# Kernel optimization log

Measured on AMD Instinct MI355X. Metric: run time of the kernel, lower is better.

Reference implementation:

```python
import jax, jax.numpy as jnp
import numpy as np

B, N, DIM = 4, 4096, 1024
HEADS, DIM_HEAD, M = 16, 64, 128
DIM_INNER = HEADS * DIM_HEAD
SCALE = DIM_HEAD ** -0.5


def setup_inputs() -> dict:
    key = jax.random.key(0)
    ks = jax.random.split(key, 7)
    x = jax.random.normal(ks[0], (B, N, DIM), dtype=jnp.float32)
    mask = jax.random.bernoulli(ks[1], 0.9, (B, N))  # bool [b, n]
    W_qkv = jax.random.normal(ks[2], (DIM, 3 * DIM_INNER), dtype=jnp.float32) * (DIM ** -0.5)
    agent_tokens = jax.random.normal(ks[3], (HEADS, M, DIM_HEAD), dtype=jnp.float32) * 0.02
    W_qa = jax.random.normal(ks[4], (HEADS, HEADS), dtype=jnp.float32) * (HEADS ** -0.5)
    W_ak = jax.random.normal(ks[5], (HEADS, HEADS), dtype=jnp.float32) * (HEADS ** -0.5)
    W_out = jax.random.normal(ks[6], (DIM_INNER, DIM), dtype=jnp.float32) * (DIM_INNER ** -0.5)
    return {"x": x, "mask": mask, "W_qkv": W_qkv, "agent_tokens": agent_tokens,
            "W_qa": W_qa, "W_ak": W_ak, "W_out": W_out}


def reference(x, mask, W_qkv, agent_tokens, W_qa, W_ak, W_out):
    b, n, _ = x.shape
    h, m, d = agent_tokens.shape
    # qkv projection -> [3, b, h, n, d]  (layout matches 'b n (qkv h d)')
    qkv = (x @ W_qkv).reshape(b, n, 3, h, d).transpose(2, 0, 3, 1, 4)
    q, k, v = qkv[0], qkv[1], qkv[2]
    a = agent_tokens * SCALE  # [h, m, d]
    # stage 1: query-agent similarities [b, h, n, m]
    qa_sim = jnp.einsum('bhid,hjd->bhij', q, a)
    # stage 2: agent-key similarities [b, h, m, n]
    ak_sim = jnp.einsum('hid,bhjd->bhij', a, k)
    max_neg = -jnp.finfo(ak_sim.dtype).max
    ak_sim = jnp.where(mask[:, None, None, :], ak_sim, max_neg)
    qa_attn = jax.nn.softmax(qa_sim, axis=-1)
    ak_attn = jax.nn.softmax(ak_sim, axis=-1)
    # talking heads: 1x1 conv over head dim == head-mixing matmul
    qa_attn = jnp.einsum('gh,bhij->bgij', W_qa, qa_attn)
    ak_attn = jnp.einsum('gh,bhij->bgij', W_ak, ak_attn)
    agent_out = jnp.einsum('bhmn,bhnd->bhmd', ak_attn, v)    # [b, h, m, d]
    out = jnp.einsum('bhnm,bhmd->bhnd', qa_attn, agent_out)  # [b, h, n, d]
    out = jnp.where(mask[:, None, :, None], out, 0.0)
    out = out.transpose(0, 2, 1, 3).reshape(b, n, h * d)
    return out @ W_out
```

## Files before the change

kernel.cpp:

```cpp
#include <hip/hip_runtime.h>
#include <stdint.h>

#define DEVI __device__ __forceinline__

typedef __bf16 bf16x8 __attribute__((ext_vector_type(8)));
typedef float  f32x4  __attribute__((ext_vector_type(4)));
typedef unsigned int u32x2 __attribute__((ext_vector_type(2)));


DEVI unsigned short f2bf(float f) {
  union { float f; unsigned int u; } c; c.f = f;
  return (unsigned short)((c.u + 0x7fffu + ((c.u >> 16) & 1u)) >> 16);
}
DEVI float bf2f(unsigned short s) {
  union { unsigned int u; float f; } c; c.u = ((unsigned int)s) << 16;
  return c.f;
}
DEVI u32x2 pack4(float a, float b, float c, float d) {
  u32x2 r;
  r.x = (unsigned)f2bf(a) | ((unsigned)f2bf(b) << 16);
  r.y = (unsigned)f2bf(c) | ((unsigned)f2bf(d) << 16);
  return r;
}
DEVI bf16x8 ldg8(const unsigned short* p) { return *(const bf16x8*)p; }

DEVI void g2l16(const void* g, void* l) {
  __builtin_amdgcn_global_load_lds(
      (const __attribute__((address_space(1))) unsigned int*)g,
      (__attribute__((address_space(3))) unsigned int*)l, 16, 0, 0);
}

#define MFMA16(acc, a, b) acc = __builtin_amdgcn_mfma_f32_16x16x32_bf16((a), (b), (acc), 0, 0, 0)

#define VMCNT8() asm volatile("s_waitcnt vmcnt(8)")
#define VMCNT0() asm volatile("s_waitcnt vmcnt(0)")
#define LGKM0()  asm volatile("s_waitcnt lgkmcnt(0)")
#define SBAR()   __builtin_amdgcn_s_barrier()

__global__ __launch_bounds__(256) void k_prep(
    const float* __restrict__ x, const float* __restrict__ Wqkv,
    const float* __restrict__ ag, const float* __restrict__ Wout,
    unsigned short* __restrict__ Xb, unsigned short* __restrict__ WqkvT,
    unsigned short* __restrict__ Ab, unsigned short* __restrict__ WoT,
    float* __restrict__ rowsum)
{
  __shared__ float ldsT[32][33];
  const int tid = threadIdx.x;
  int bx = blockIdx.x;
  if (bx < 16384) {
    size_t i4 = ((size_t)bx * 256 + tid) * 4;
    f32x4 v = *(const f32x4*)&x[i4];
    *(u32x2*)&Xb[i4] = pack4(v[0], v[1], v[2], v[3]);
    return;
  }
  bx -= 16384;
  if (bx < 3072) {
    int jt = bx % 96, kt = bx / 96;
    int r32 = tid >> 3, c4 = (tid & 7) * 4;
    f32x4 v = *(const f32x4*)&Wqkv[(size_t)(kt * 32 + r32) * 3072 + jt * 32 + c4];
#pragma unroll
    for (int i = 0; i < 4; i++) ldsT[r32][c4 + i] = v[i];
    __syncthreads();
    float o0 = ldsT[c4 + 0][r32], o1 = ldsT[c4 + 1][r32];
    float o2 = ldsT[c4 + 2][r32], o3 = ldsT[c4 + 3][r32];
    *(u32x2*)&WqkvT[(size_t)(jt * 32 + r32) * 1024 + kt * 32 + c4] = pack4(o0, o1, o2, o3);
    return;
  }
  bx -= 3072;
  if (bx < 128) {
    size_t i4 = ((size_t)bx * 256 + tid) * 4;
    f32x4 v = *(const f32x4*)&ag[i4];
    *(u32x2*)&Ab[i4] = pack4(v[0] * 0.125f, v[1] * 0.125f, v[2] * 0.125f, v[3] * 0.125f);
    return;
  }
  bx -= 128;
  if (bx < 1024) {
    int ct = bx % 32, dt = bx / 32;
    int r32 = tid >> 3, c4 = (tid & 7) * 4;
    f32x4 v = *(const f32x4*)&Wout[(size_t)(dt * 32 + r32) * 1024 + ct * 32 + c4];
#pragma unroll
    for (int i = 0; i < 4; i++) ldsT[r32][c4 + i] = v[i];
    __syncthreads();
    float o0 = ldsT[c4 + 0][r32], o1 = ldsT[c4 + 1][r32];
    float o2 = ldsT[c4 + 2][r32], o3 = ldsT[c4 + 3][r32];
    *(u32x2*)&WoT[(size_t)(ct * 32 + r32) * 1024 + dt * 32 + c4] = pack4(o0, o1, o2, o3);
    return;
  }
  bx -= 1024;
  {
    const f32x4 z = {0.f, 0.f, 0.f, 0.f};
    *(f32x4*)&rowsum[((size_t)bx * 256 + tid) * 4] = z;
  }
}

DEVI void gemm_core_256(const unsigned short* __restrict__ A,
                        const unsigned short* __restrict__ Bt,
                        int row0, int col0, int swap,
                        unsigned short* ldsS, f32x4 acc[8][4])
{
  const int tid = threadIdx.x, lane = tid & 63, w = tid >> 6;
  const int q = lane >> 4, r = lane & 15;
  const int wm = w >> 2, wn = w & 3;
  const int abA = swap ? 2 : 0, abB = swap ? 0 : 2;
  const int afhalf = wm, bvhalf = wn >> 1;
  const int afr = r * 64;
  const int bvr = ((wn & 1) * 64 + r) * 64;
  const int cs0 = (q ^ (r & 7)) << 3;
  const int cs1 = ((q + 4) ^ (r & 7)) << 3;
  const int gr = tid >> 3;
  const int gcol = ((tid & 7) ^ ((tid >> 3) & 7)) << 3;
  const unsigned short* gA = A + (size_t)(row0 + gr) * 1024 + gcol;
  const unsigned short* gB = Bt + (size_t)(col0 + gr) * 1024 + gcol;
  const int ldst = w * 512;

  const f32x4 z = {0.f, 0.f, 0.f, 0.f};
#pragma unroll
  for (int i = 0; i < 8; i++)
#pragma unroll
    for (int j = 0; j < 4; j++) acc[i][j] = z;

  auto stageH = [&](const unsigned short* G, int half, int koff, int slot) {
    const unsigned short* g0 = G + (size_t)half * 131072 + koff;
    g2l16(g0, ldsS + slot + ldst);
    g2l16(g0 + 65536, ldsS + slot + 4096 + ldst);
  };

#pragma unroll
  for (int s = 0; s < 2; ++s) {
    stageH(gB, 0, s * 64, ((s << 2) | 2 | 0) << 13);
    stageH(gB, 1, s * 64, ((s << 2) | 2 | 1) << 13);
    stageH(gA, 0, s * 64, ((s << 2) | 0 | 0) << 13);
    stageH(gA, 1, s * 64, ((s << 2) | 0 | 1) << 13);
  }
  VMCNT8();
  SBAR();

  auto kstep = [&](const int P, const int s) {
    const int afb = (((P << 2) | abA | afhalf) << 13) + afr;
    const int bvb = (((P << 2) | abB | bvhalf) << 13) + bvr;
    bf16x8 af[4][2], bva[2][2], bvx[2][2];
#pragma unroll
    for (int rt = 0; rt < 4; rt++) {
      af[rt][0] = *(const bf16x8*)&ldsS[afb + rt * 1024 + cs0];
      af[rt][1] = *(const bf16x8*)&ldsS[afb + rt * 1024 + cs1];
    }
#pragma unroll
    for (int ct = 0; ct < 2; ct++) {
      bva[ct][0] = *(const bf16x8*)&ldsS[bvb + ct * 1024 + cs0];
      bva[ct][1] = *(const bf16x8*)&ldsS[bvb + ct * 1024 + cs1];
    }
    SBAR(); LGKM0();
    __builtin_amdgcn_s_setprio(1);
#pragma unroll
    for (int rt = 0; rt < 4; rt++)
#pragma unroll
      for (int ct = 0; ct < 2; ct++) {
        MFMA16(acc[rt][ct], af[rt][0], bva[ct][0]);
        MFMA16(acc[rt][ct], af[rt][1], bva[ct][1]);
      }
    __builtin_amdgcn_s_setprio(0);
    SBAR();
#pragma unroll
    for (int ct = 0; ct < 2; ct++) {
      bvx[ct][0] = *(const bf16x8*)&ldsS[bvb + (ct + 2) * 1024 + cs0];
      bvx[ct][1] = *(const bf16x8*)&ldsS[bvb + (ct + 2) * 1024 + cs1];
    }
    SBAR(); LGKM0();
    __builtin_amdgcn_s_setprio(1);
#pragma unroll
    for (int rt = 0; rt < 4; rt++)
#pragma unroll
      for (int ct = 0; ct < 2; ct++) {
        MFMA16(acc[rt][ct + 2], af[rt][0], bvx[ct][0]);
        MFMA16(acc[rt][ct + 2], af[rt][1], bvx[ct][1]);
      }
    __builtin_amdgcn_s_setprio(0);
    SBAR();
#pragma unroll
    for (int rt = 0; rt < 4; rt++) {
      af[rt][0] = *(const bf16x8*)&ldsS[afb + (rt + 4) * 1024 + cs0];
      af[rt][1] = *(const bf16x8*)&ldsS[afb + (rt + 4) * 1024 + cs1];
    }
    if (s < 14) {
      stageH(gB, 0, (s + 2) * 64, ((P << 2) | 2 | 0) << 13);
      stageH(gB, 1, (s + 2) * 64, ((P << 2) | 2 | 1) << 13);
    }
    SBAR(); LGKM0();
    __builtin_amdgcn_s_setprio(1);
#pragma unroll
    for (int rt = 0; rt < 4; rt++)
#pragma unroll
      for (int ct = 0; ct < 2; ct++) {
        MFMA16(acc[rt + 4][ct], af[rt][0], bva[ct][0]);
        MFMA16(acc[rt + 4][ct], af[rt][1], bva[ct][1]);
      }
    __builtin_amdgcn_s_setprio(0);
    SBAR();
    if (s < 14) {
      stageH(gA, 0, (s + 2) * 64, ((P << 2) | 0 | 0) << 13);
      stageH(gA, 1, (s + 2) * 64, ((P << 2) | 0 | 1) << 13);
      VMCNT8();
    } else if (s == 14) {
      VMCNT0();
    }
    SBAR(); LGKM0();
    __builtin_amdgcn_s_setprio(1);
#pragma unroll
    for (int rt = 0; rt < 4; rt++)
#pragma unroll
      for (int ct = 0; ct < 2; ct++) {
        MFMA16(acc[rt + 4][ct + 2], af[rt][0], bvx[ct][0]);
        MFMA16(acc[rt + 4][ct + 2], af[rt][1], bvx[ct][1]);
      }
    __builtin_amdgcn_s_setprio(0);
    SBAR();
  };

  for (int it = 0; it < 8; ++it) {
    kstep(0, 2 * it);
    kstep(1, 2 * it + 1);
  }
}

__global__ __launch_bounds__(512, 2) void k_gemm_qkv(
    const unsigned short* __restrict__ A, const unsigned short* __restrict__ Bt,
    unsigned short* __restrict__ Q, unsigned short* __restrict__ Kd,
    unsigned short* __restrict__ Vt)
{
  __shared__ __align__(16) unsigned short lds[65536];
  const int tid = threadIdx.x, lane = tid & 63, w = tid >> 6;
  const int q = lane >> 4, r = lane & 15, wm = w >> 2, wn = w & 3;
  const int row0 = blockIdx.x * 256, col0 = blockIdx.y * 256;
  const bool qk = blockIdx.y < 8;

  f32x4 acc[8][4];
  gemm_core_256(A, Bt, row0, col0, qk ? 1 : 0, lds, acc);

  const int b = row0 >> 12, row0b = row0 & 4095;
  if (qk) {
    unsigned short* dst = (col0 < 1024) ? Q : Kd;
    const int jb = (col0 & 1023) + wm * 128;
#pragma unroll
    for (int rt = 0; rt < 8; rt++)
#pragma unroll
      for (int ct = 0; ct < 4; ct++) {
        int j = jb + rt * 16 + 4 * q;
        int h = j >> 6, d0 = j & 63;
        int n = row0b + wn * 64 + ct * 16 + r;
        u32x2 pk = pack4(acc[rt][ct][0], acc[rt][ct][1], acc[rt][ct][2], acc[rt][ct][3]);
        *(u32x2*)&dst[(((size_t)(b * 16 + h)) * 4096 + n) * 64 + d0] = pk;
      }
  } else {
    const int jb = (col0 - 2048) + wn * 64;
#pragma unroll
    for (int rt = 0; rt < 8; rt++)
#pragma unroll
      for (int ct = 0; ct < 4; ct++) {
        int j = jb + ct * 16 + r;
        int h = j >> 6, d = j & 63;
        int n = row0b + wm * 128 + rt * 16 + 4 * q;
        u32x2 pk = pack4(acc[rt][ct][0], acc[rt][ct][1], acc[rt][ct][2], acc[rt][ct][3]);
        *(u32x2*)&Vt[(((size_t)(b * 16 + h)) * 64 + d) * 4096 + n] = pk;
      }
  }
}

__global__ __launch_bounds__(256, 2) void k_qk(
    const unsigned short* __restrict__ Q, const unsigned short* __restrict__ Kd,
    const unsigned short* __restrict__ Ab, const int* __restrict__ mask,
    unsigned short* __restrict__ QA, unsigned short* __restrict__ E,
    float* __restrict__ rowsum)
{
  const int tid = threadIdx.x, lane = tid & 63, w = tid >> 6;
  const int q = lane >> 4, r = lane & 15, wr = w >> 1, wc = w & 1;
  const int nt = blockIdx.x, h = blockIdx.y, b = blockIdx.z;
  const unsigned short* Qb = Q + (((size_t)(b * 16 + h)) * 4096 + nt * 128) * 64;
  const unsigned short* Kb = Kd + (((size_t)(b * 16 + h)) * 4096 + nt * 128) * 64;
  const unsigned short* Ah = Ab + (size_t)h * 8192;
  __shared__ float rs[2][128];
  const f32x4 z = {0.f, 0.f, 0.f, 0.f};

  {
    f32x4 acc[4][4];
#pragma unroll
    for (int i = 0; i < 4; i++)
#pragma unroll
      for (int j = 0; j < 4; j++) acc[i][j] = z;
#pragma unroll
    for (int ks = 0; ks < 2; ks++) {
      bf16x8 af[4], bv[4];
#pragma unroll
      for (int rt = 0; rt < 4; rt++) af[rt] = ldg8(Ah + (size_t)(64 * wr + 16 * rt + r) * 64 + ks * 32 + q * 8);
#pragma unroll
      for (int ct = 0; ct < 4; ct++) bv[ct] = ldg8(Qb + (size_t)(64 * wc + 16 * ct + r) * 64 + ks * 32 + q * 8);
#pragma unroll
      for (int rt = 0; rt < 4; rt++)
#pragma unroll
        for (int ct = 0; ct < 4; ct++) MFMA16(acc[rt][ct], af[rt], bv[ct]);
    }
    float cs[4];
#pragma unroll
    for (int ct = 0; ct < 4; ct++) {
      float s = 0.f;
#pragma unroll
      for (int rt = 0; rt < 4; rt++)
#pragma unroll
        for (int reg = 0; reg < 4; reg++) {
          float e = __expf(acc[rt][ct][reg]);
          acc[rt][ct][reg] = e; s += e;
        }
      s += __shfl_xor(s, 16); s += __shfl_xor(s, 32);
      cs[ct] = s;
    }
    if (q == 0) {
#pragma unroll
      for (int ct = 0; ct < 4; ct++) rs[wr][64 * wc + 16 * ct + r] = cs[ct];
    }
    __syncthreads();
#pragma unroll
    for (int ct = 0; ct < 4; ct++) {
      int nl = 64 * wc + 16 * ct + r;
      float inv = 1.0f / (rs[0][nl] + rs[1][nl]);
      int n = nt * 128 + nl;
      size_t base = (((size_t)(b * 16 + h)) * 4096 + n) * 128;
#pragma unroll
      for (int rt = 0; rt < 4; rt++) {
        int m0 = 64 * wr + 16 * rt + 4 * q;
        u32x2 pk = pack4(acc[rt][ct][0] * inv, acc[rt][ct][1] * inv,
                         acc[rt][ct][2] * inv, acc[rt][ct][3] * inv);
        *(u32x2*)&QA[base + m0] = pk;
      }
    }
  }
  __syncthreads();

  {
    f32x4 acc[4][4];
#pragma unroll
    for (int i = 0; i < 4; i++)
#pragma unroll
      for (int j = 0; j < 4; j++) acc[i][j] = z;
#pragma unroll
    for (int ks = 0; ks < 2; ks++) {
      bf16x8 af[4], bv[4];
#pragma unroll
      for (int rt = 0; rt < 4; rt++) af[rt] = ldg8(Kb + (size_t)(64 * wr + 16 * rt + r) * 64 + ks * 32 + q * 8);
#pragma unroll
      for (int ct = 0; ct < 4; ct++) bv[ct] = ldg8(Ah + (size_t)(64 * wc + 16 * ct + r) * 64 + ks * 32 + q * 8);
#pragma unroll
      for (int rt = 0; rt < 4; rt++)
#pragma unroll
        for (int ct = 0; ct < 4; ct++) MFMA16(acc[rt][ct], af[rt], bv[ct]);
    }
    float cs[4] = {0.f, 0.f, 0.f, 0.f};
#pragma unroll
    for (int rt = 0; rt < 4; rt++) {
      const int4 mkv = *(const int4*)&mask[b * 4096 + nt * 128 + 64 * wr + 16 * rt + 4 * q];
      int mka[4] = {mkv.x, mkv.y, mkv.z, mkv.w};
#pragma unroll
      for (int ct = 0; ct < 4; ct++) {
#pragma unroll
        for (int reg = 0; reg < 4; reg++) {
          float e = mka[reg] ? __expf(acc[rt][ct][reg]) : 0.0f;
          acc[rt][ct][reg] = e; cs[ct] += e;
        }
      }
    }
#pragma unroll
    for (int ct = 0; ct < 4; ct++) {
      float s = cs[ct];
      s += __shfl_xor(s, 16); s += __shfl_xor(s, 32);
      cs[ct] = s;
    }
    if (q == 0) {
#pragma unroll
      for (int ct = 0; ct < 4; ct++) rs[wr][64 * wc + 16 * ct + r] = cs[ct];
    }
#pragma unroll
    for (int ct = 0; ct < 4; ct++) {
      int m = 64 * wc + 16 * ct + r;
      size_t base = (((size_t)(b * 16 + h)) * 128 + m) * 4096;
#pragma unroll
      for (int rt = 0; rt < 4; rt++) {
        int n0 = nt * 128 + 64 * wr + 16 * rt + 4 * q;
        u32x2 pk = pack4(acc[rt][ct][0], acc[rt][ct][1], acc[rt][ct][2], acc[rt][ct][3]);
        *(u32x2*)&E[base + n0] = pk;
      }
    }
    __syncthreads();
    if (tid < 128) atomicAdd(&rowsum[(b * 16 + h) * 128 + tid], rs[0][tid] + rs[1][tid]);
  }
}

__global__ __launch_bounds__(256) void k_mix(
    const unsigned short* __restrict__ E, const float* __restrict__ rowsum,
    const float* __restrict__ Wak, unsigned short* __restrict__ MIX)
{
  const int tid = threadIdx.x;
  const int m = blockIdx.y, b = blockIdx.z;
  __shared__ float wv[256];
  __shared__ float inv[16];
  wv[tid] = Wak[tid];
  if (tid < 16) inv[tid] = 1.0f / rowsum[(b * 16 + tid) * 128 + m];
  __syncthreads();
  const int n0 = (blockIdx.x * 256 + tid) * 4;
  float p[16][4];
#pragma unroll
  for (int h = 0; h < 16; h++) {
    u32x2 v = *(const u32x2*)&E[(((size_t)(b * 16 + h)) * 128 + m) * 4096 + n0];
    float iv = inv[h];
    p[h][0] = bf2f((unsigned short)(v.x & 0xffff)) * iv;
    p[h][1] = bf2f((unsigned short)(v.x >> 16)) * iv;
    p[h][2] = bf2f((unsigned short)(v.y & 0xffff)) * iv;
    p[h][3] = bf2f((unsigned short)(v.y >> 16)) * iv;
  }
#pragma unroll
  for (int g = 0; g < 16; g++) {
    float s0 = 0.f, s1 = 0.f, s2 = 0.f, s3 = 0.f;
#pragma unroll
    for (int h = 0; h < 16; h++) {
      float wgh = wv[g * 16 + h];
      s0 += wgh * p[h][0]; s1 += wgh * p[h][1]; s2 += wgh * p[h][2]; s3 += wgh * p[h][3];
    }
    *(u32x2*)&MIX[(((size_t)(b * 16 + g)) * 128 + m) * 4096 + n0] = pack4(s0, s1, s2, s3);
  }
}

__global__ __launch_bounds__(256) void k_ao(
    const unsigned short* __restrict__ MIX, const unsigned short* __restrict__ Vt,
    float* __restrict__ P)
{
  const int tid = threadIdx.x, lane = tid & 63, w4 = tid >> 6;
  const int q = lane >> 4, r = lane & 15;
  const int kc = blockIdx.x, g = blockIdx.y, b = blockIdx.z;
  const unsigned short* Abase = MIX + ((size_t)(b * 16 + g)) * 128 * 4096;
  const unsigned short* Bbase = Vt + ((size_t)(b * 16 + g)) * 64 * 4096;
  f32x4 acc[2][4];
  const f32x4 z = {0.f, 0.f, 0.f, 0.f};
#pragma unroll
  for (int i = 0; i < 2; i++)
#pragma unroll
    for (int j = 0; j < 4; j++) acc[i][j] = z;
  for (int n = kc * 512; n < kc * 512 + 512; n += 32) {
    bf16x8 af[2], bv[4];
#pragma unroll
    for (int rt = 0; rt < 2; rt++) af[rt] = ldg8(Abase + (size_t)(32 * w4 + 16 * rt + r) * 4096 + n + q * 8);
#pragma unroll
    for (int ct = 0; ct < 4; ct++) bv[ct] = ldg8(Bbase + (size_t)(16 * ct + r) * 4096 + n + q * 8);
#pragma unroll
    for (int rt = 0; rt < 2; rt++)
#pragma unroll
      for (int ct = 0; ct < 4; ct++) MFMA16(acc[rt][ct], af[rt], bv[ct]);
  }
  float* Pp = P + (size_t)kc * 524288 + ((size_t)(b * 16 + g)) * 8192;
#pragma unroll
  for (int rt = 0; rt < 2; rt++)
#pragma unroll
    for (int ct = 0; ct < 4; ct++) {
      int m0 = 32 * w4 + 16 * rt + 4 * q, d = 16 * ct + r;
      *(f32x4*)&Pp[(size_t)d * 128 + m0] = acc[rt][ct];
    }
}

__global__ __launch_bounds__(256) void k_aored(
    const float* __restrict__ P, float* __restrict__ AOt)
{
  size_t i = ((size_t)blockIdx.x * 256 + threadIdx.x) * 4;
  f32x4 s = *(const f32x4*)&P[i];
#pragma unroll
  for (int kc = 1; kc < 8; kc++) {
    f32x4 v = *(const f32x4*)&P[(size_t)kc * 524288 + i];
    s[0] += v[0]; s[1] += v[1]; s[2] += v[2]; s[3] += v[3];
  }
  *(f32x4*)&AOt[i] = s;
}

__global__ __launch_bounds__(256) void k_mixqa(
    const unsigned short* __restrict__ QA, const float* __restrict__ Wqa,
    unsigned short* __restrict__ QAmix)
{
  const int tid = threadIdx.x;
  const int b = blockIdx.y;
  __shared__ float wv[256];
  wv[tid] = Wqa[tid];
  __syncthreads();
  const size_t i0 = ((size_t)blockIdx.x * 256 + tid) * 4;
  float p[16][4];
#pragma unroll
  for (int h = 0; h < 16; h++) {
    u32x2 v = *(const u32x2*)&QA[((size_t)(b * 16 + h)) * 524288 + i0];
    p[h][0] = bf2f((unsigned short)(v.x & 0xffff));
    p[h][1] = bf2f((unsigned short)(v.x >> 16));
    p[h][2] = bf2f((unsigned short)(v.y & 0xffff));
    p[h][3] = bf2f((unsigned short)(v.y >> 16));
  }
#pragma unroll
  for (int g = 0; g < 16; g++) {
    float s0 = 0.f, s1 = 0.f, s2 = 0.f, s3 = 0.f;
#pragma unroll
    for (int h = 0; h < 16; h++) {
      float wgh = wv[g * 16 + h];
      s0 += wgh * p[h][0]; s1 += wgh * p[h][1]; s2 += wgh * p[h][2]; s3 += wgh * p[h][3];
    }
    *(u32x2*)&QAmix[((size_t)(b * 16 + g)) * 524288 + i0] = pack4(s0, s1, s2, s3);
  }
}

__global__ __launch_bounds__(256) void k_o1(
    const unsigned short* __restrict__ QAmix, const float* __restrict__ AOt,
    unsigned short* __restrict__ out1)
{
  const int tid = threadIdx.x, lane = tid & 63, w4 = tid >> 6;
  const int q = lane >> 4, r = lane & 15;
  const int nt = blockIdx.x, g = blockIdx.y, b = blockIdx.z;
  const unsigned short* Bbase = QAmix + (((size_t)(b * 16 + g)) * 4096 + nt * 128) * 128;
  const float* Abase = AOt + ((size_t)(b * 16 + g)) * 8192;
  f32x4 acc[4][2];
  const f32x4 z = {0.f, 0.f, 0.f, 0.f};
#pragma unroll
  for (int i = 0; i < 4; i++)
#pragma unroll
    for (int j = 0; j < 2; j++) acc[i][j] = z;
#pragma unroll
  for (int ks = 0; ks < 4; ks++) {
    bf16x8 af[4], bv[2];
#pragma unroll
    for (int rt = 0; rt < 4; rt++) {
      const float* p = Abase + (size_t)(16 * rt + r) * 128 + ks * 32 + q * 8;
      f32x4 f0 = *(const f32x4*)p;
      f32x4 f1 = *(const f32x4*)(p + 4);
      bf16x8 t;
#pragma unroll
      for (int jj = 0; jj < 4; jj++) { t[jj] = (__bf16)f0[jj]; t[4 + jj] = (__bf16)f1[jj]; }
      af[rt] = t;
    }
#pragma unroll
    for (int ct = 0; ct < 2; ct++)
      bv[ct] = ldg8(Bbase + (size_t)(32 * w4 + 16 * ct + r) * 128 + ks * 32 + q * 8);
#pragma unroll
    for (int rt = 0; rt < 4; rt++)
#pragma unroll
      for (int ct = 0; ct < 2; ct++) MFMA16(acc[rt][ct], af[rt], bv[ct]);
  }
#pragma unroll
  for (int ct = 0; ct < 2; ct++) {
    int n = nt * 128 + 32 * w4 + 16 * ct + r;
    size_t base = ((size_t)b * 4096 + n) * 1024 + g * 64;
#pragma unroll
    for (int rt = 0; rt < 4; rt++) {
      int d0 = 16 * rt + 4 * q;
      u32x2 pk = pack4(acc[rt][ct][0], acc[rt][ct][1], acc[rt][ct][2], acc[rt][ct][3]);
      *(u32x2*)&out1[base + d0] = pk;
    }
  }
}

__global__ __launch_bounds__(512, 2) void k_fin2(
    const unsigned short* __restrict__ A, const unsigned short* __restrict__ Bt,
    const int* __restrict__ mask, float* __restrict__ out)
{
  __shared__ __align__(16) unsigned short lds[65536];
  const int tid = threadIdx.x, lane = tid & 63, w = tid >> 6;
  const int q = lane >> 4, r = lane & 15, wm = w >> 2, wn = w & 3;
  const int row0 = blockIdx.x * 256, col0 = blockIdx.y * 256;

  f32x4 acc[8][4];
  gemm_core_256(A, Bt, row0, col0, 0, lds, acc);

#pragma unroll
  for (int rt = 0; rt < 8; rt++) {
    const int4 mkv = *(const int4*)&mask[row0 + wm * 128 + rt * 16 + 4 * q];
    int mka[4] = {mkv.x, mkv.y, mkv.z, mkv.w};
#pragma unroll
    for (int reg = 0; reg < 4; reg++) {
      int row = row0 + wm * 128 + rt * 16 + 4 * q + reg;
#pragma unroll
      for (int ct = 0; ct < 4; ct++) {
        int c = col0 + wn * 64 + ct * 16 + r;
        out[(size_t)row * 1024 + c] = mka[reg] ? acc[rt][ct][reg] : 0.0f;
      }
    }
  }
}

extern "C" void kernel_launch(void* const* d_in, const int* in_sizes, int n_in,
                              void* d_out, int out_size, void* d_ws, size_t ws_size,
                              hipStream_t stream) {
  const float* x    = (const float*)d_in[0];
  const int*   mask = (const int*)d_in[1];
  const float* Wqkv = (const float*)d_in[2];
  const float* ag   = (const float*)d_in[3];
  const float* Wqa  = (const float*)d_in[4];
  const float* Wak  = (const float*)d_in[5];
  const float* Wout = (const float*)d_in[6];
  float* out = (float*)d_out;
  char* ws = (char*)d_ws;

  unsigned short* QA    = (unsigned short*)(ws + 0);
  unsigned short* QQ    = (unsigned short*)(ws + 67108864);
  unsigned short* KK    = (unsigned short*)(ws + 67108864 + 33554432);
  unsigned short* MIX   = QQ;
  unsigned short* out1  = QQ;
  unsigned short* VT    = (unsigned short*)(ws + 134217728);
  unsigned short* Xb    = (unsigned short*)(ws + 167772160);
  unsigned short* WqkvT = (unsigned short*)(ws + 167772160 + 33554432);
  unsigned short* E     = Xb;
  float*          Ppart = (float*)Xb;
  unsigned short* QAmix = Xb;
  char* sm = ws + 234881024;
  unsigned short* Ab  = (unsigned short*)(sm);
  unsigned short* WoT = (unsigned short*)(sm + 262144);
  float* rowsum = (float*)(sm + 262144 + 2097152);
  float* AOt    = (float*)(sm + 262144 + 2097152 + 32768);

  k_prep<<<20616, 256, 0, stream>>>(x, Wqkv, ag, Wout, Xb, WqkvT, Ab, WoT, rowsum);
  k_gemm_qkv<<<dim3(64, 12), 512, 0, stream>>>(Xb, WqkvT, QQ, KK, VT);
  k_qk<<<dim3(32, 16, 4), 256, 0, stream>>>(QQ, KK, Ab, mask, QA, E, rowsum);
  k_mix<<<dim3(4, 128, 4), 256, 0, stream>>>(E, rowsum, Wak, MIX);
  k_ao<<<dim3(8, 16, 4), 256, 0, stream>>>(MIX, VT, Ppart);
  k_aored<<<512, 256, 0, stream>>>(Ppart, AOt);
  k_mixqa<<<dim3(512, 4), 256, 0, stream>>>(QA, Wqa, QAmix);
  k_o1<<<dim3(32, 16, 4), 256, 0, stream>>>(QAmix, AOt, out1);
  k_fin2<<<dim3(64, 4), 512, 0, stream>>>(out1, WoT, mask, out);
}
```

Before: 462.8 us.

## Fuse query-agent softmax with talking-heads mix into one kernel

Adds a new kernel that computes the query-agent similarities for all 16 heads of a 32-row tile, applies the softmax, keeps the bf16 probabilities in registers, and applies the W_qa head mix before writing QAmix. This removes the separate k_mixqa pass and the write and re-read of the 64 MB intermediate QA buffer. k_qk now only handles the agent-key branch. The fused kernel keeps a large register array (16x2x2 packed values plus accumulators), which may lower occupancy. It also needs two block barriers per head and launches only 512 blocks.

```diff
diff --git a/kernel.cpp b/kernel.cpp
--- a/kernel.cpp
+++ b/kernel.cpp
@@ -265,131 +265,181 @@
   }
 }
 
+__global__ __launch_bounds__(256, 2) void k_qamix(
+    const unsigned short* __restrict__ Q, const unsigned short* __restrict__ Ab,
+    const float* __restrict__ Wqa, unsigned short* __restrict__ QAmix)
+{
+  const int tid = threadIdx.x, lane = tid & 63, w = tid >> 6;
+  const int q = lane >> 4, r = lane & 15;
+  const int nt = blockIdx.x, b = blockIdx.y;
+  __shared__ float wq[256];
+  __shared__ float rsq[4][32];
+  wq[tid] = Wqa[tid];
+  __syncthreads();
+
+  const f32x4 z = {0.f, 0.f, 0.f, 0.f};
+  u32x2 p[16][2][2];
+
+#pragma unroll
+  for (int h = 0; h < 16; ++h) {
+    const unsigned short* Qb = Q + (((size_t)(b * 16 + h)) * 4096 + nt * 32) * 64;
+    const unsigned short* Ah = Ab + (size_t)h * 8192;
+    f32x4 acc[2][2];
+    acc[0][0] = z; acc[0][1] = z; acc[1][0] = z; acc[1][1] = z;
+#pragma unroll
+    for (int ks = 0; ks < 2; ++ks) {
+      bf16x8 af[2], bv[2];
+#pragma unroll
+      for (int rt = 0; rt < 2; rt++) af[rt] = ldg8(Ah + (size_t)(32 * w + 16 * rt + r) * 64 + ks * 32 + q * 8);
+#pragma unroll
+      for (int ct = 0; ct < 2; ct++) bv[ct] = ldg8(Qb + (size_t)(16 * ct + r) * 64 + ks * 32 + q * 8);
+#pragma unroll
+      for (int rt = 0; rt < 2; rt++)
+#pragma unroll
+        for (int ct = 0; ct < 2; ct++) MFMA16(acc[rt][ct], af[rt], bv[ct]);
+    }
+    float e[2][2][4];
+    float s0 = 0.f, s1 = 0.f;
+#pragma unroll
+    for (int rt = 0; rt < 2; rt++)
+#pragma unroll
+      for (int reg = 0; reg < 4; reg++) {
+        float e0 = __expf(acc[rt][0][reg]); e[rt][0][reg] = e0; s0 += e0;
+        float e1 = __expf(acc[rt][1][reg]); e[rt][1][reg] = e1; s1 += e1;
+      }
+    s0 += __shfl_xor(s0, 16); s0 += __shfl_xor(s0, 32);
+    s1 += __shfl_xor(s1, 16); s1 += __shfl_xor(s1, 32);
+    if (lane < 16) { rsq[w][r] = s0; rsq[w][16 + r] = s1; }
+    __syncthreads();
+    float invv[2];
+#pragma unroll
+    for (int ct = 0; ct < 2; ct++) {
+      int n = 16 * ct + r;
+      invv[ct] = 1.0f / (rsq[0][n] + rsq[1][n] + rsq[2][n] + rsq[3][n]);
+    }
+#pragma unroll
+    for (int rt = 0; rt < 2; rt++)
+#pragma unroll
+      for (int ct = 0; ct < 2; ct++)
+        p[h][rt][ct] = pack4(e[rt][ct][0] * invv[ct], e[rt][ct][1] * invv[ct],
+                             e[rt][ct][2] * invv[ct], e[rt][ct][3] * invv[ct]);
+    __syncthreads();
+  }
+
+#pragma unroll
+  for (int gg = 0; gg < 4; ++gg) {
+    f32x4 s[4][2][2];
+#pragma unroll
+    for (int gp = 0; gp < 4; gp++) { s[gp][0][0] = z; s[gp][0][1] = z; s[gp][1][0] = z; s[gp][1][1] = z; }
+#pragma unroll
+    for (int h = 0; h < 16; ++h) {
+      float f[2][2][4];
+#pragma unroll
+      for (int rt = 0; rt < 2; rt++)
+#pragma unroll
+        for (int ct = 0; ct < 2; ct++) {
+          u32x2 v = p[h][rt][ct];
+          f[rt][ct][0] = bf2f((unsigned short)(v.x & 0xffff));
+          f[rt][ct][1] = bf2f((unsigned short)(v.x >> 16));
+          f[rt][ct][2] = bf2f((unsigned short)(v.y & 0xffff));
+          f[rt][ct][3] = bf2f((unsigned short)(v.y >> 16));
+        }
+#pragma unroll
+      for (int gp = 0; gp < 4; ++gp) {
+        float wgh = wq[(gg * 4 + gp) * 16 + h];
+#pragma unroll
+        for (int rt = 0; rt < 2; rt++)
+#pragma unroll
+          for (int ct = 0; ct < 2; ct++)
+#pragma unroll
+            for (int reg = 0; reg < 4; reg++)
+              s[gp][rt][ct][reg] += wgh * f[rt][ct][reg];
+      }
+    }
+#pragma unroll
+    for (int gp = 0; gp < 4; ++gp) {
+      int g = gg * 4 + gp;
+      size_t gbase = ((size_t)(b * 16 + g)) * 4096 + nt * 32;
+#pragma unroll
+      for (int rt = 0; rt < 2; rt++)
+#pragma unroll
+        for (int ct = 0; ct < 2; ct++) {
+          int n = 16 * ct + r, m0 = 32 * w + 16 * rt + 4 * q;
+          u32x2 pk = pack4(s[gp][rt][ct][0], s[gp][rt][ct][1],
+                           s[gp][rt][ct][2], s[gp][rt][ct][3]);
+          *(u32x2*)&QAmix[(gbase + n) * 128 + m0] = pk;
+        }
+    }
+  }
+}
+
 __global__ __launch_bounds__(256, 2) void k_qk(
-    const unsigned short* __restrict__ Q, const unsigned short* __restrict__ Kd,
-    const unsigned short* __restrict__ Ab, const int* __restrict__ mask,
-    unsigned short* __restrict__ QA, unsigned short* __restrict__ E,
+    const unsigned short* __restrict__ Kd, const unsigned short* __restrict__ Ab,
+    const int* __restrict__ mask, unsigned short* __restrict__ E,
     float* __restrict__ rowsum)
 {
   const int tid = threadIdx.x, lane = tid & 63, w = tid >> 6;
   const int q = lane >> 4, r = lane & 15, wr = w >> 1, wc = w & 1;
   const int nt = blockIdx.x, h = blockIdx.y, b = blockIdx.z;
-  const unsigned short* Qb = Q + (((size_t)(b * 16 + h)) * 4096 + nt * 128) * 64;
   const unsigned short* Kb = Kd + (((size_t)(b * 16 + h)) * 4096 + nt * 128) * 64;
   const unsigned short* Ah = Ab + (size_t)h * 8192;
   __shared__ float rs[2][128];
   const f32x4 z = {0.f, 0.f, 0.f, 0.f};
 
-  {
-    f32x4 acc[4][4];
-#pragma unroll
-    for (int i = 0; i < 4; i++)
-#pragma unroll
-      for (int j = 0; j < 4; j++) acc[i][j] = z;
-#pragma unroll
-    for (int ks = 0; ks < 2; ks++) {
-      bf16x8 af[4], bv[4];
-#pragma unroll
-      for (int rt = 0; rt < 4; rt++) af[rt] = ldg8(Ah + (size_t)(64 * wr + 16 * rt + r) * 64 + ks * 32 + q * 8);
-#pragma unroll
-      for (int ct = 0; ct < 4; ct++) bv[ct] = ldg8(Qb + (size_t)(64 * wc + 16 * ct + r) * 64 + ks * 32 + q * 8);
-#pragma unroll
-      for (int rt = 0; rt < 4; rt++)
-#pragma unroll
-        for (int ct = 0; ct < 4; ct++) MFMA16(acc[rt][ct], af[rt], bv[ct]);
-    }
-    float cs[4];
+  f32x4 acc[4][4];
+#pragma unroll
+  for (int i = 0; i < 4; i++)
+#pragma unroll
+    for (int j = 0; j < 4; j++) acc[i][j] = z;
+#pragma unroll
+  for (int ks = 0; ks < 2; ks++) {
+    bf16x8 af[4], bv[4];
+#pragma unroll
+    for (int rt = 0; rt < 4; rt++) af[rt] = ldg8(Kb + (size_t)(64 * wr + 16 * rt + r) * 64 + ks * 32 + q * 8);
+#pragma unroll
+    for (int ct = 0; ct < 4; ct++) bv[ct] = ldg8(Ah + (size_t)(64 * wc + 16 * ct + r) * 64 + ks * 32 + q * 8);
+#pragma unroll
+    for (int rt = 0; rt < 4; rt++)
+#pragma unroll
+      for (int ct = 0; ct < 4; ct++) MFMA16(acc[rt][ct], af[rt], bv[ct]);
+  }
+  float cs[4] = {0.f, 0.f, 0.f, 0.f};
+#pragma unroll
+  for (int rt = 0; rt < 4; rt++) {
+    const int4 mkv = *(const int4*)&mask[b * 4096 + nt * 128 + 64 * wr + 16 * rt + 4 * q];
+    int mka[4] = {mkv.x, mkv.y, mkv.z, mkv.w};
 #pragma unroll
     for (int ct = 0; ct < 4; ct++) {
-      float s = 0.f;
-#pragma unroll
-      for (int rt = 0; rt < 4; rt++)
-#pragma unroll
-        for (int reg = 0; reg < 4; reg++) {
-          float e = __expf(acc[rt][ct][reg]);
-          acc[rt][ct][reg] = e; s += e;
-        }
-      s += __shfl_xor(s, 16); s += __shfl_xor(s, 32);
-      cs[ct] = s;
-    }
-    if (q == 0) {
-#pragma unroll
-      for (int ct = 0; ct < 4; ct++) rs[wr][64 * wc + 16 * ct + r] = cs[ct];
-    }
-    __syncthreads();
-#pragma unroll
-    for (int ct = 0; ct < 4; ct++) {
-      int nl = 64 * wc + 16 * ct + r;
-      float inv = 1.0f / (rs[0][nl] + rs[1][nl]);
-      int n = nt * 128 + nl;
-      size_t base = (((size_t)(b * 16 + h)) * 4096 + n) * 128;
-#pragma unroll
-      for (int rt = 0; rt < 4; rt++) {
-        int m0 = 64 * wr + 16 * rt + 4 * q;
-        u32x2 pk = pack4(acc[rt][ct][0] * inv, acc[rt][ct][1] * inv,
-                         acc[rt][ct][2] * inv, acc[rt][ct][3] * inv);
-        *(u32x2*)&QA[base + m0] = pk;
-      }
+#pragma unroll
+      for (int reg = 0; reg < 4; reg++) {
+        float e = mka[reg] ? __expf(acc[rt][ct][reg]) : 0.0f;
+        acc[rt][ct][reg] = e; cs[ct] += e;
+      }
+    }
+  }
+#pragma unroll
+  for (int ct = 0; ct < 4; ct++) {
+    float s = cs[ct];
+    s += __shfl_xor(s, 16); s += __shfl_xor(s, 32);
+    cs[ct] = s;
+  }
+  if (q == 0) {
+#pragma unroll
+    for (int ct = 0; ct < 4; ct++) rs[wr][64 * wc + 16 * ct + r] = cs[ct];
+  }
+#pragma unroll
+  for (int ct = 0; ct < 4; ct++) {
+    int m = 64 * wc + 16 * ct + r;
+    size_t base = (((size_t)(b * 16 + h)) * 128 + m) * 4096;
+#pragma unroll
+    for (int rt = 0; rt < 4; rt++) {
+      int n0 = nt * 128 + 64 * wr + 16 * rt + 4 * q;
+      u32x2 pk = pack4(acc[rt][ct][0], acc[rt][ct][1], acc[rt][ct][2], acc[rt][ct][3]);
+      *(u32x2*)&E[base + n0] = pk;
     }
   }
   __syncthreads();
-
-  {
-    f32x4 acc[4][4];
-#pragma unroll
-    for (int i = 0; i < 4; i++)
-#pragma unroll
-      for (int j = 0; j < 4; j++) acc[i][j] = z;
-#pragma unroll
-    for (int ks = 0; ks < 2; ks++) {
-      bf16x8 af[4], bv[4];
-#pragma unroll
-      for (int rt = 0; rt < 4; rt++) af[rt] = ldg8(Kb + (size_t)(64 * wr + 16 * rt + r) * 64 + ks * 32 + q * 8);
-#pragma unroll
-      for (int ct = 0; ct < 4; ct++) bv[ct] = ldg8(Ah + (size_t)(64 * wc + 16 * ct + r) * 64 + ks * 32 + q * 8);
-#pragma unroll
-      for (int rt = 0; rt < 4; rt++)
-#pragma unroll
-        for (int ct = 0; ct < 4; ct++) MFMA16(acc[rt][ct], af[rt], bv[ct]);
-    }
-    float cs[4] = {0.f, 0.f, 0.f, 0.f};
-#pragma unroll
-    for (int rt = 0; rt < 4; rt++) {
-      const int4 mkv = *(const int4*)&mask[b * 4096 + nt * 128 + 64 * wr + 16 * rt + 4 * q];
-      int mka[4] = {mkv.x, mkv.y, mkv.z, mkv.w};
-#pragma unroll
-      for (int ct = 0; ct < 4; ct++) {
-#pragma unroll
-        for (int reg = 0; reg < 4; reg++) {
-          float e = mka[reg] ? __expf(acc[rt][ct][reg]) : 0.0f;
-          acc[rt][ct][reg] = e; cs[ct] += e;
-        }
-      }
-    }
-#pragma unroll
-    for (int ct = 0; ct < 4; ct++) {
-      float s = cs[ct];
-      s += __shfl_xor(s, 16); s += __shfl_xor(s, 32);
-      cs[ct] = s;
-    }
-    if (q == 0) {
-#pragma unroll
-      for (int ct = 0; ct < 4; ct++) rs[wr][64 * wc + 16 * ct + r] = cs[ct];
-    }
-#pragma unroll
-    for (int ct = 0; ct < 4; ct++) {
-      int m = 64 * wc + 16 * ct + r;
-      size_t base = (((size_t)(b * 16 + h)) * 128 + m) * 4096;
-#pragma unroll
-      for (int rt = 0; rt < 4; rt++) {
-        int n0 = nt * 128 + 64 * wr + 16 * rt + 4 * q;
-        u32x2 pk = pack4(acc[rt][ct][0], acc[rt][ct][1], acc[rt][ct][2], acc[rt][ct][3]);
-        *(u32x2*)&E[base + n0] = pk;
-      }
-    }
-    __syncthreads();
-    if (tid < 128) atomicAdd(&rowsum[(b * 16 + h) * 128 + tid], rs[0][tid] + rs[1][tid]);
-  }
+  if (tid < 128) atomicAdd(&rowsum[(b * 16 + h) * 128 + tid], rs[0][tid] + rs[1][tid]);
 }
 
 __global__ __launch_bounds__(256) void k_mix(
@@ -473,37 +523,6 @@
     s[0] += v[0]; s[1] += v[1]; s[2] += v[2]; s[3] += v[3];
   }
   *(f32x4*)&AOt[i] = s;
-}
-
-__global__ __launch_bounds__(256) void k_mixqa(
-    const unsigned short* __restrict__ QA, const float* __restrict__ Wqa,
-    unsigned short* __restrict__ QAmix)
-{
-  const int tid = threadIdx.x;
-  const int b = blockIdx.y;
-  __shared__ float wv[256];
-  wv[tid] = Wqa[tid];
-  __syncthreads();
-  const size_t i0 = ((size_t)blockIdx.x * 256 + tid) * 4;
-  float p[16][4];
-#pragma unroll
-  for (int h = 0; h < 16; h++) {
-    u32x2 v = *(const u32x2*)&QA[((size_t)(b * 16 + h)) * 524288 + i0];
-    p[h][0] = bf2f((unsigned short)(v.x & 0xffff));
-    p[h][1] = bf2f((unsigned short)(v.x >> 16));
-    p[h][2] = bf2f((unsigned short)(v.y & 0xffff));
-    p[h][3] = bf2f((unsigned short)(v.y >> 16));
-  }
-#pragma unroll
-  for (int g = 0; g < 16; g++) {
-    float s0 = 0.f, s1 = 0.f, s2 = 0.f, s3 = 0.f;
-#pragma unroll
-    for (int h = 0; h < 16; h++) {
-      float wgh = wv[g * 16 + h];
-      s0 += wgh * p[h][0]; s1 += wgh * p[h][1]; s2 += wgh * p[h][2]; s3 += wgh * p[h][3];
-    }
-    *(u32x2*)&QAmix[((size_t)(b * 16 + g)) * 524288 + i0] = pack4(s0, s1, s2, s3);
-  }
 }
 
 __global__ __launch_bounds__(256) void k_o1(
@@ -596,7 +615,7 @@
   float* out = (float*)d_out;
   char* ws = (char*)d_ws;
 
-  unsigned short* QA    = (unsigned short*)(ws + 0);
+  unsigned short* QAmix = (unsigned short*)(ws + 0);
   unsigned short* QQ    = (unsigned short*)(ws + 67108864);
   unsigned short* KK    = (unsigned short*)(ws + 67108864 + 33554432);
   unsigned short* MIX   = QQ;
@@ -606,7 +625,6 @@
   unsigned short* WqkvT = (unsigned short*)(ws + 167772160 + 33554432);
   unsigned short* E     = Xb;
   float*          Ppart = (float*)Xb;
-  unsigned short* QAmix = Xb;
   char* sm = ws + 234881024;
   unsigned short* Ab  = (unsigned short*)(sm);
   unsigned short* WoT = (unsigned short*)(sm + 262144);
@@ -615,11 +633,11 @@
 
   k_prep<<<20616, 256, 0, stream>>>(x, Wqkv, ag, Wout, Xb, WqkvT, Ab, WoT, rowsum);
   k_gemm_qkv<<<dim3(64, 12), 512, 0, stream>>>(Xb, WqkvT, QQ, KK, VT);
-  k_qk<<<dim3(32, 16, 4), 256, 0, stream>>>(QQ, KK, Ab, mask, QA, E, rowsum);
+  k_qamix<<<dim3(128, 4), 256, 0, stream>>>(QQ, Ab, Wqa, QAmix);
+  k_qk<<<dim3(32, 16, 4), 256, 0, stream>>>(KK, Ab, mask, E, rowsum);
   k_mix<<<dim3(4, 128, 4), 256, 0, stream>>>(E, rowsum, Wak, MIX);
   k_ao<<<dim3(8, 16, 4), 256, 0, stream>>>(MIX, VT, Ppart);
   k_aored<<<512, 256, 0, stream>>>(Ppart, AOt);
-  k_mixqa<<<dim3(512, 4), 256, 0, stream>>>(QA, Wqa, QAmix);
   k_o1<<<dim3(32, 16, 4), 256, 0, stream>>>(QAmix, AOt, out1);
   k_fin2<<<dim3(64, 4), 512, 0, stream>>>(out1, WoT, mask, out);
 }
```

Result: slower. 635.7 us (+37.4%).

## Fuse query-agent head mixing into the output matmul via LDS staging

Applied to the files above, without the earlier changes.

Merges the talking-heads mixing kernel for query-agent attention with the following agent-output matmul. Each block loads 16 rows of QA for all heads into LDS, mixes across heads in registers, writes the mixed bf16 tile to padded LDS, and each wave then runs MFMAs for four heads. This removes the global round-trip of the 128MB QAmix intermediate and one launch. The cost is large LDS use (about 1 block per CU), a smaller 16-row tile per head, and AOt being reloaded and converted to bf16 once per 16 rows, which is more often than before.

```diff
diff --git a/kernel.cpp b/kernel.cpp
--- a/kernel.cpp
+++ b/kernel.cpp
@@ -475,81 +475,91 @@
   *(f32x4*)&AOt[i] = s;
 }
 
-__global__ __launch_bounds__(256) void k_mixqa(
+__global__ __launch_bounds__(256, 1) void k_mo(
     const unsigned short* __restrict__ QA, const float* __restrict__ Wqa,
-    unsigned short* __restrict__ QAmix)
-{
-  const int tid = threadIdx.x;
-  const int b = blockIdx.y;
+    const float* __restrict__ AOt, unsigned short* __restrict__ out1)
+{
+  __shared__ __align__(16) unsigned short pL[16 * 2048];
+  __shared__ __align__(16) unsigned short qam[16 * 2176];
   __shared__ float wv[256];
+  const int tid = threadIdx.x, lane = tid & 63, w = tid >> 6;
+  const int q = lane >> 4, r = lane & 15;
+  const int nt = blockIdx.x, b = blockIdx.y;
   wv[tid] = Wqa[tid];
+
+  const unsigned short* gq = QA + ((size_t)b * 16) * 524288 + nt * 2048 + w * 512 + lane * 8;
+#pragma unroll
+  for (int h = 0; h < 16; ++h)
+    g2l16(gq + (size_t)h * 524288, pL + h * 2048 + w * 512);
+  VMCNT0();
   __syncthreads();
-  const size_t i0 = ((size_t)blockIdx.x * 256 + tid) * 4;
-  float p[16][4];
-#pragma unroll
-  for (int h = 0; h < 16; h++) {
-    u32x2 v = *(const u32x2*)&QA[((size_t)(b * 16 + h)) * 524288 + i0];
-    p[h][0] = bf2f((unsigned short)(v.x & 0xffff));
-    p[h][1] = bf2f((unsigned short)(v.x >> 16));
-    p[h][2] = bf2f((unsigned short)(v.y & 0xffff));
-    p[h][3] = bf2f((unsigned short)(v.y >> 16));
-  }
-#pragma unroll
-  for (int g = 0; g < 16; g++) {
-    float s0 = 0.f, s1 = 0.f, s2 = 0.f, s3 = 0.f;
-#pragma unroll
-    for (int h = 0; h < 16; h++) {
-      float wgh = wv[g * 16 + h];
-      s0 += wgh * p[h][0]; s1 += wgh * p[h][1]; s2 += wgh * p[h][2]; s3 += wgh * p[h][3];
-    }
-    *(u32x2*)&QAmix[((size_t)(b * 16 + g)) * 524288 + i0] = pack4(s0, s1, s2, s3);
-  }
-}
-
-__global__ __launch_bounds__(256) void k_o1(
-    const unsigned short* __restrict__ QAmix, const float* __restrict__ AOt,
-    unsigned short* __restrict__ out1)
-{
-  const int tid = threadIdx.x, lane = tid & 63, w4 = tid >> 6;
-  const int q = lane >> 4, r = lane & 15;
-  const int nt = blockIdx.x, g = blockIdx.y, b = blockIdx.z;
-  const unsigned short* Bbase = QAmix + (((size_t)(b * 16 + g)) * 4096 + nt * 128) * 128;
-  const float* Abase = AOt + ((size_t)(b * 16 + g)) * 8192;
-  f32x4 acc[4][2];
+
+  const int myoff = tid * 8;
+  const int n_ = tid >> 4, m8 = (tid & 15) * 8;
+#pragma unroll
+  for (int gc = 0; gc < 4; ++gc) {
+    float s[4][8];
+#pragma unroll
+    for (int gp = 0; gp < 4; gp++)
+#pragma unroll
+      for (int j = 0; j < 8; j++) s[gp][j] = 0.f;
+#pragma unroll
+    for (int h = 0; h < 16; ++h) {
+      const u32x2 v0 = *(const u32x2*)&pL[h * 2048 + myoff];
+      const u32x2 v1 = *(const u32x2*)&pL[h * 2048 + myoff + 4];
+      float f[8];
+      f[0] = bf2f((unsigned short)(v0.x & 0xffff)); f[1] = bf2f((unsigned short)(v0.x >> 16));
+      f[2] = bf2f((unsigned short)(v0.y & 0xffff)); f[3] = bf2f((unsigned short)(v0.y >> 16));
+      f[4] = bf2f((unsigned short)(v1.x & 0xffff)); f[5] = bf2f((unsigned short)(v1.x >> 16));
+      f[6] = bf2f((unsigned short)(v1.y & 0xffff)); f[7] = bf2f((unsigned short)(v1.y >> 16));
+#pragma unroll
+      for (int gp = 0; gp < 4; ++gp) {
+        float wgh = wv[(gc * 4 + gp) * 16 + h];
+#pragma unroll
+        for (int j = 0; j < 8; j++) s[gp][j] += wgh * f[j];
+      }
+    }
+#pragma unroll
+    for (int gp = 0; gp < 4; ++gp) {
+      int g = gc * 4 + gp;
+      *(u32x2*)&qam[g * 2176 + n_ * 136 + m8] = pack4(s[gp][0], s[gp][1], s[gp][2], s[gp][3]);
+      *(u32x2*)&qam[g * 2176 + n_ * 136 + m8 + 4] = pack4(s[gp][4], s[gp][5], s[gp][6], s[gp][7]);
+    }
+  }
+  __syncthreads();
+
   const f32x4 z = {0.f, 0.f, 0.f, 0.f};
 #pragma unroll
-  for (int i = 0; i < 4; i++)
-#pragma unroll
-    for (int j = 0; j < 2; j++) acc[i][j] = z;
-#pragma unroll
-  for (int ks = 0; ks < 4; ks++) {
-    bf16x8 af[4], bv[2];
-#pragma unroll
-    for (int rt = 0; rt < 4; rt++) {
-      const float* p = Abase + (size_t)(16 * rt + r) * 128 + ks * 32 + q * 8;
-      f32x4 f0 = *(const f32x4*)p;
-      f32x4 f1 = *(const f32x4*)(p + 4);
-      bf16x8 t;
-#pragma unroll
-      for (int jj = 0; jj < 4; jj++) { t[jj] = (__bf16)f0[jj]; t[4 + jj] = (__bf16)f1[jj]; }
-      af[rt] = t;
-    }
-#pragma unroll
-    for (int ct = 0; ct < 2; ct++)
-      bv[ct] = ldg8(Bbase + (size_t)(32 * w4 + 16 * ct + r) * 128 + ks * 32 + q * 8);
-#pragma unroll
-    for (int rt = 0; rt < 4; rt++)
-#pragma unroll
-      for (int ct = 0; ct < 2; ct++) MFMA16(acc[rt][ct], af[rt], bv[ct]);
-  }
-#pragma unroll
-  for (int ct = 0; ct < 2; ct++) {
-    int n = nt * 128 + 32 * w4 + 16 * ct + r;
+  for (int gi = 0; gi < 4; ++gi) {
+    const int g = w * 4 + gi;
+    const float* Ag = AOt + ((size_t)(b * 16 + g)) * 8192;
+    const unsigned short* Bg = &qam[g * 2176];
+    f32x4 acc[4];
+#pragma unroll
+    for (int i = 0; i < 4; i++) acc[i] = z;
+#pragma unroll
+    for (int ks = 0; ks < 4; ++ks) {
+      bf16x8 af[4], bv;
+#pragma unroll
+      for (int rt = 0; rt < 4; rt++) {
+        const float* p = Ag + (size_t)(16 * rt + r) * 128 + ks * 32 + q * 8;
+        f32x4 f0 = *(const f32x4*)p;
+        f32x4 f1 = *(const f32x4*)(p + 4);
+        bf16x8 t;
+#pragma unroll
+        for (int jj = 0; jj < 4; jj++) { t[jj] = (__bf16)f0[jj]; t[4 + jj] = (__bf16)f1[jj]; }
+        af[rt] = t;
+      }
+      bv = *(const bf16x8*)&Bg[r * 136 + ks * 32 + q * 8];
+#pragma unroll
+      for (int rt = 0; rt < 4; rt++) MFMA16(acc[rt], af[rt], bv);
+    }
+    int n = nt * 16 + r;
     size_t base = ((size_t)b * 4096 + n) * 1024 + g * 64;
 #pragma unroll
     for (int rt = 0; rt < 4; rt++) {
       int d0 = 16 * rt + 4 * q;
-      u32x2 pk = pack4(acc[rt][ct][0], acc[rt][ct][1], acc[rt][ct][2], acc[rt][ct][3]);
+      u32x2 pk = pack4(acc[rt][0], acc[rt][1], acc[rt][2], acc[rt][3]);
       *(u32x2*)&out1[base + d0] = pk;
     }
   }
@@ -606,7 +616,6 @@
   unsigned short* WqkvT = (unsigned short*)(ws + 167772160 + 33554432);
   unsigned short* E     = Xb;
   float*          Ppart = (float*)Xb;
-  unsigned short* QAmix = Xb;
   char* sm = ws + 234881024;
   unsigned short* Ab  = (unsigned short*)(sm);
   unsigned short* WoT = (unsigned short*)(sm + 262144);
@@ -619,7 +628,6 @@
   k_mix<<<dim3(4, 128, 4), 256, 0, stream>>>(E, rowsum, Wak, MIX);
   k_ao<<<dim3(8, 16, 4), 256, 0, stream>>>(MIX, VT, Ppart);
   k_aored<<<512, 256, 0, stream>>>(Ppart, AOt);
-  k_mixqa<<<dim3(512, 4), 256, 0, stream>>>(QA, Wqa, QAmix);
-  k_o1<<<dim3(32, 16, 4), 256, 0, stream>>>(QAmix, AOt, out1);
+  k_mo<<<dim3(256, 4), 256, 0, stream>>>(QA, Wqa, AOt, out1);
   k_fin2<<<dim3(64, 4), 512, 0, stream>>>(out1, WoT, mask, out);
 }
```

New measurement: 495.8 us. +7.1%, slower.
